# Performance work log

Measured on AMD Instinct MI355X. Metric: run time of the kernel, lower is better.

## Reference

```python
import jax, jax.numpy as jnp
import numpy as np

N_CYCLES = 20000  # number of cycles in the cycle basis (segments)


def setup_inputs() -> dict:
    key = jax.random.key(0)
    k1, k2, k3, k4, k5 = jax.random.split(key, 5)
    B, NB, E = 256, 50000, 160000  # batch, n_branches, total cycle-basis entries
    c = jax.random.normal(k1, (B, NB), dtype=jnp.float32)
    s = jax.random.normal(k2, (B, NB), dtype=jnp.float32)
    # signs are +/-1
    cysigns = jnp.where(jax.random.uniform(k4, (E,)) < 0.5, -1.0, 1.0).astype(jnp.float32)
    cyinds = jax.random.randint(k3, (E,), 0, NB, dtype=jnp.int32)
    # from_value_rowids requires nondecreasing row ids
    cyrows = jnp.sort(jax.random.randint(k5, (E,), 0, N_CYCLES, dtype=jnp.int32))
    return {"c": c, "s": s, "cysigns": cysigns, "cyinds": cyinds, "cyrows": cyrows}


def reference(c, s, cysigns, cyinds, cyrows):
    # gather branch vars per cycle-basis entry: [B, E]
    cg = jnp.take(c, cyinds, axis=1)
    sg = cysigns * jnp.take(s, cyinds, axis=1)
    # tf.math.angle(tf.complex(rc, rs)) == atan2(imag, real)
    ang = jnp.arctan2(sg, cg)  # [B, E]
    # ragged per-cycle sum == segment_sum over the entry axis -> [N_CYCLES, B]
    v_kvl = jax.ops.segment_sum(ang.T, cyrows, num_segments=N_CYCLES)
    # scalar KVL violation
    return jnp.mean(jnp.abs(v_kvl))
```

## Files before the change

### kernel.cpp

```cpp
#include <hip/hip_runtime.h>

#define NB     50000
#define NB4    12500
#define BATCH  256
#define NCYC   20000
#define QSCALE  (127.0f / 3.14159265358979f)
#define DQSCALE (3.14159265358979f / 127.0f)
#define OUTSCALE (1.0f / ((float)NCYC * (float)BATCH))

__device__ __forceinline__ float fast_atan2q(float y, float x) {
    const float ax = __builtin_fabsf(x);
    const float ay = __builtin_fabsf(y);
    const float mx = fmaxf(ax, ay);
    const float mn = fminf(ax, ay);
    const float t  = mn * __builtin_amdgcn_rcpf(mx);
    const float t2 = t * t;
    float p = fmaf(t2, fmaf(t2, fmaf(t2, fmaf(t2,
                  0.84219761f, -3.44137383f), 7.28200966f), -13.35163894f),
                  40.42416382f);
    p *= t;
    p = (ay > ax) ? (63.5f - p) : p;
    p = (x < 0.0f) ? (127.0f - p) : p;
    return copysignf(p, y);
}

__device__ __forceinline__ unsigned int q8(float y, float x) {
    return (unsigned int)(unsigned char)(signed char)__float2int_rn(fast_atan2q(y, x));
}

__global__ __launch_bounds__(256) void theta_k(
        const float4* __restrict__ c4, const float4* __restrict__ s4,
        signed char* __restrict__ th, int* __restrict__ row_start,
        const int* __restrict__ rows, int E) {
    const int u = threadIdx.x;
    if (blockIdx.y == 0) {
        const int g = blockIdx.x * 256 + u;
        if (g <= NCYC) {
            int lo = 0, hi = E;
            while (lo < hi) { const int m = (lo + hi) >> 1; if (rows[m] < g) lo = m + 1; else hi = m; }
            row_start[g] = lo;
        }
    }

    const int lane = u & 63;
    const int w    = u >> 6;
    const int x4   = blockIdx.x * 64 + lane;
    if (x4 >= NB4) return;
    const int b0   = blockIdx.y * 64 + 16 * w;

    unsigned int pw[16];
    #pragma unroll
    for (int r = 0; r < 16; ++r) {
        const float4 vc = c4[(size_t)(b0 + r) * NB4 + x4];
        const float4 vs = s4[(size_t)(b0 + r) * NB4 + x4];
        pw[r] =  q8(vs.x, vc.x)
              | (q8(vs.y, vc.y) << 8)
              | (q8(vs.z, vc.z) << 16)
              | (q8(vs.w, vc.w) << 24);
    }

    #pragma unroll
    for (int j = 0; j < 4; ++j) {
        uint4 o;
        unsigned int* op = &o.x;
        #pragma unroll
        for (int q = 0; q < 4; ++q) {
            const unsigned int sh = 8 * j;
            op[q] =  ((pw[4 * q + 0] >> sh) & 0xffu)
                  | (((pw[4 * q + 1] >> sh) & 0xffu) << 8)
                  | (((pw[4 * q + 2] >> sh) & 0xffu) << 16)
                  | (((pw[4 * q + 3] >> sh) & 0xffu) << 24);
        }
        const int nb = 4 * x4 + j;
        *reinterpret_cast<uint4*>(&th[(size_t)nb * BATCH + b0]) = o;
    }
}

__global__ __launch_bounds__(256) void kvl3_k(
        const signed char* __restrict__ th,
        const float* __restrict__ signs, const int* __restrict__ inds,
        const int* __restrict__ row_start,
        float* __restrict__ partials) {
    __shared__ float wsum[4];
    const int tid  = threadIdx.x;
    const int wave = tid >> 6;
    const int lane = tid & 63;
    const int r    = blockIdx.x * 4 + wave;
    const int start = row_start[r];
    const int end   = row_start[r + 1];

    float a0 = 0.f, a1 = 0.f, a2 = 0.f, a3 = 0.f;
    int e = start;
    for (; e + 2 <= end; e += 2) {
        const int   i0 = inds[e],  i1 = inds[e + 1];
        const float g0 = signs[e] * DQSCALE, g1 = signs[e + 1] * DQSCALE;
        const unsigned int u0 = *reinterpret_cast<const unsigned int*>(&th[(size_t)i0 * BATCH + lane * 4]);
        const unsigned int u1 = *reinterpret_cast<const unsigned int*>(&th[(size_t)i1 * BATCH + lane * 4]);
        a0 += g0 * (float)(signed char)(u0      ) + g1 * (float)(signed char)(u1      );
        a1 += g0 * (float)(signed char)(u0 >>  8) + g1 * (float)(signed char)(u1 >>  8);
        a2 += g0 * (float)(signed char)(u0 >> 16) + g1 * (float)(signed char)(u1 >> 16);
        a3 += g0 * (float)(signed char)(u0 >> 24) + g1 * (float)(signed char)(u1 >> 24);
    }
    if (e < end) {
        const float g0 = signs[e] * DQSCALE;
        const unsigned int u0 = *reinterpret_cast<const unsigned int*>(&th[(size_t)inds[e] * BATCH + lane * 4]);
        a0 += g0 * (float)(signed char)(u0      );
        a1 += g0 * (float)(signed char)(u0 >>  8);
        a2 += g0 * (float)(signed char)(u0 >> 16);
        a3 += g0 * (float)(signed char)(u0 >> 24);
    }
    float v = fabsf(a0) + fabsf(a1) + fabsf(a2) + fabsf(a3);
    #pragma unroll
    for (int off = 32; off > 0; off >>= 1)
        v += __shfl_down(v, off, 64);
    if (lane == 0) wsum[wave] = v;
    __syncthreads();
    if (tid == 0)
        partials[blockIdx.x] = wsum[0] + wsum[1] + wsum[2] + wsum[3];
}

__global__ __launch_bounds__(1024) void reduce_k(
        const float* __restrict__ partials, float* __restrict__ out) {
    const int tid = threadIdx.x;
    float v = 0.f;
    for (int i = tid; i < NCYC / 4; i += 1024) v += partials[i];
    #pragma unroll
    for (int off = 32; off > 0; off >>= 1)
        v += __shfl_down(v, off, 64);
    __shared__ float wsum[16];
    if ((tid & 63) == 0) wsum[tid >> 6] = v;
    __syncthreads();
    if (tid == 0) {
        float t = 0.f;
        #pragma unroll
        for (int w = 0; w < 16; ++w) t += wsum[w];
        out[0] = t * OUTSCALE;
    }
}

__global__ void zero_out_k(float* out) { if (threadIdx.x == 0) out[0] = 0.0f; }

__global__ __launch_bounds__(256) void kvl_fallback_k(
        const float* __restrict__ c, const float* __restrict__ s,
        const float* __restrict__ signs, const int* __restrict__ inds,
        const int* __restrict__ rows, int E, float* __restrict__ out) {
    const int r = blockIdx.x;
    int lo = 0, hi = E;
    while (lo < hi) { const int m = (lo + hi) >> 1; if (rows[m] < r) lo = m + 1; else hi = m; }
    const int start = lo;
    hi = E;
    while (lo < hi) { const int m = (lo + hi) >> 1; if (rows[m] <= r) lo = m + 1; else hi = m; }
    const int end = lo;
    const int tid = threadIdx.x;
    float acc = 0.f;
    for (int e = start; e < end; ++e) {
        const int idx = inds[e];
        const float sg = signs[e];
        acc += atan2f(sg * s[(size_t)tid * NB + idx], c[(size_t)tid * NB + idx]);
    }
    float v = fabsf(acc);
    #pragma unroll
    for (int off = 32; off > 0; off >>= 1)
        v += __shfl_down(v, off, 64);
    __shared__ float wsum[4];
    if ((tid & 63) == 0) wsum[tid >> 6] = v;
    __syncthreads();
    if (tid == 0)
        atomicAdd(out, (wsum[0] + wsum[1] + wsum[2] + wsum[3]) *
                       (1.0f / ((float)NCYC * (float)BATCH)));
}

extern "C" void kernel_launch(void* const* d_in, const int* in_sizes, int n_in,
                              void* d_out, int out_size, void* d_ws, size_t ws_size,
                              hipStream_t stream) {
    const float* c       = (const float*)d_in[0];
    const float* s       = (const float*)d_in[1];
    const float* cysigns = (const float*)d_in[2];
    const int*   cyinds  = (const int*)d_in[3];
    const int*   cyrows  = (const int*)d_in[4];
    const int    E       = in_sizes[2];
    float* out = (float*)d_out;

    const size_t th_bytes = (size_t)NB * BATCH;
    const size_t rs_bytes = (size_t)(NCYC + 1) * sizeof(int);
    const size_t pa_bytes = (size_t)(NCYC / 4) * sizeof(float);
    const size_t need = th_bytes + rs_bytes + pa_bytes;
    if (ws_size >= need) {
        signed char* th   = (signed char*)d_ws;
        int* row_start    = (int*)(th + th_bytes);
        float* partials   = (float*)((char*)row_start + rs_bytes);

        dim3 tg((NB4 + 63) / 64, BATCH / 64);
        theta_k<<<tg, 256, 0, stream>>>((const float4*)c, (const float4*)s,
                                        th, row_start, cyrows, E);
        kvl3_k<<<NCYC / 4, 256, 0, stream>>>(th, cysigns, cyinds, row_start,
                                             partials);
        reduce_k<<<1, 1024, 0, stream>>>(partials, out);
    } else {
        zero_out_k<<<1, 64, 0, stream>>>(out);
        kvl_fallback_k<<<NCYC, 256, 0, stream>>>(c, s, cysigns, cyinds, cyrows, E, out);
    }
}
```

Before: 156.5 us.

## Stage theta inputs through LDS with direct global-to-LDS loads and transpose

The theta kernel now loads 16 batch rows of c and s per block straight into shared memory using the global_load_lds builtin, then has each thread compute one branch's 16 quantized angles from LDS. Each thread stores one 16-byte vector, replacing the old in-register byte shuffling across 64 batch rows. The grid grows from 4 to 16 blocks along batch, which adds parallelism but gives each thread less work and adds a block barrier. The direct-to-LDS load and the assumed LDS layout (each wave's 64 lanes filling one contiguous row) rely on specific hardware behaviour.

```diff
diff --git a/kernel.cpp b/kernel.cpp
--- a/kernel.cpp
+++ b/kernel.cpp
@@ -28,11 +28,21 @@
     return (unsigned int)(unsigned char)(signed char)__float2int_rn(fast_atan2q(y, x));
 }
 
+__device__ __forceinline__ void gload16(const void* g, void* l) {
+    __builtin_amdgcn_global_load_lds(
+        (const __attribute__((address_space(1))) void*)g,
+        (__attribute__((address_space(3))) void*)l,
+        16, 0, 0);
+}
+
 __global__ __launch_bounds__(256) void theta_k(
         const float4* __restrict__ c4, const float4* __restrict__ s4,
         signed char* __restrict__ th, int* __restrict__ row_start,
         const int* __restrict__ rows, int E) {
+    __shared__ float4 ct[16][64];
+    __shared__ float4 st[16][64];
     const int u = threadIdx.x;
+
     if (blockIdx.y == 0) {
         const int g = blockIdx.x * 256 + u;
         if (g <= NCYC) {
@@ -42,37 +52,35 @@
         }
     }
 
-    const int lane = u & 63;
-    const int w    = u >> 6;
-    const int x4   = blockIdx.x * 64 + lane;
-    if (x4 >= NB4) return;
-    const int b0   = blockIdx.y * 64 + 16 * w;
-
-    unsigned int pw[16];
+    const int lane  = u & 63;
+    const int w     = u >> 6;
+    const int brow0 = blockIdx.y * 16;
+    int col = blockIdx.x * 64 + lane;
+    if (col > NB4 - 1) col = NB4 - 1;
+
+    #pragma unroll
+    for (int i = 0; i < 4; ++i) {
+        const int r = 4 * w + i;
+        gload16(&c4[(size_t)(brow0 + r) * NB4 + col], &ct[r][0]);
+        gload16(&s4[(size_t)(brow0 + r) * NB4 + col], &st[r][0]);
+    }
+    __syncthreads();
+
+    const float* cf = reinterpret_cast<const float*>(ct);
+    const float* sf = reinterpret_cast<const float*>(st);
+    unsigned int wv[4] = {0u, 0u, 0u, 0u};
     #pragma unroll
     for (int r = 0; r < 16; ++r) {
-        const float4 vc = c4[(size_t)(b0 + r) * NB4 + x4];
-        const float4 vs = s4[(size_t)(b0 + r) * NB4 + x4];
-        pw[r] =  q8(vs.x, vc.x)
-              | (q8(vs.y, vc.y) << 8)
-              | (q8(vs.z, vc.z) << 16)
-              | (q8(vs.w, vc.w) << 24);
-    }
-
-    #pragma unroll
-    for (int j = 0; j < 4; ++j) {
+        const float cc = cf[r * 256 + u];
+        const float ss = sf[r * 256 + u];
+        wv[r >> 2] |= q8(ss, cc) << (8 * (r & 3));
+    }
+
+    const int nbg = blockIdx.x * 256 + u;
+    if (nbg < NB) {
         uint4 o;
-        unsigned int* op = &o.x;
-        #pragma unroll
-        for (int q = 0; q < 4; ++q) {
-            const unsigned int sh = 8 * j;
-            op[q] =  ((pw[4 * q + 0] >> sh) & 0xffu)
-                  | (((pw[4 * q + 1] >> sh) & 0xffu) << 8)
-                  | (((pw[4 * q + 2] >> sh) & 0xffu) << 16)
-                  | (((pw[4 * q + 3] >> sh) & 0xffu) << 24);
-        }
-        const int nb = 4 * x4 + j;
-        *reinterpret_cast<uint4*>(&th[(size_t)nb * BATCH + b0]) = o;
+        o.x = wv[0]; o.y = wv[1]; o.z = wv[2]; o.w = wv[3];
+        *reinterpret_cast<uint4*>(&th[(size_t)nbg * BATCH + brow0]) = o;
     }
 }
 
@@ -190,7 +198,7 @@
         int* row_start    = (int*)(th + th_bytes);
         float* partials   = (float*)((char*)row_start + rs_bytes);
 
-        dim3 tg((NB4 + 63) / 64, BATCH / 64);
+        dim3 tg((NB4 + 63) / 64, 16);
         theta_k<<<tg, 256, 0, stream>>>((const float4*)c, (const float4*)s,
                                         th, row_start, cyrows, E);
         kvl3_k<<<NCYC / 4, 256, 0, stream>>>(th, cysigns, cyinds, row_start,
```

Result: faster. 152.7 us (-2.4%).
